# Kernel optimization log

Measured on AMD Instinct MI355X. Metric: run time of the kernel, lower is better.

## Reference

```python
import jax, jax.numpy as jnp
import numpy as np

B, H, D = 32, 64, 128          # batch (decode), indexer heads, head dim
PAGE, PAGES = 64, 128          # cache page size, pages per sequence
S = PAGE * PAGES               # max kv len = 8192
NUM_PAGES = B * PAGES          # 4096 pages total
TOPK = 2048
SCALE = float(D) ** -0.5
FILL = -1


def setup_inputs() -> dict:
    key = jax.random.key(0)
    ks = jax.random.split(key, 6)
    q = jax.random.normal(ks[0], (B, H, D), dtype=jnp.float32)
    k = jax.random.normal(ks[1], (B, D), dtype=jnp.float32)          # current-step key
    weights = jax.random.uniform(ks[2], (B, H), dtype=jnp.float32)   # per-head gates
    # fp8 cache emulated as quantized values (k_cache) x per-token scales (k_s_cache)
    k_cache = jax.random.normal(ks[3], (NUM_PAGES, PAGE, D), dtype=jnp.float32)
    k_s_cache = jax.random.uniform(ks[4], (NUM_PAGES, PAGE), minval=0.5, maxval=1.5, dtype=jnp.float32)
    kv_seqlens = jax.random.randint(ks[5], (B,), S // 2, S + 1, dtype=jnp.int32)
    block_offsets = jnp.arange(NUM_PAGES, dtype=jnp.int32).reshape(B, PAGES)
    return dict(q=q, k=k, weights=weights, k_cache=k_cache, k_s_cache=k_s_cache,
                kv_seqlens=kv_seqlens, block_offsets=block_offsets)


def reference(q, k, weights, k_cache, k_s_cache, kv_seqlens, block_offsets):
    # Gather paged cache per sequence and dequantize: [B, S, D]
    kv = k_cache[block_offsets].reshape(B, S, D) * k_s_cache[block_offsets].reshape(B, S, 1)
    pos = jnp.arange(S, dtype=jnp.int32)
    # Current step's key lives at position kv_len - 1
    cur = pos[None, :] == (kv_seqlens[:, None] - 1)
    kv = jnp.where(cur[..., None], k[:, None, :], kv)
    # Indexer score: sum_h w[b,h] * relu(q[b,h] . k[b,s]) * scale
    logits = jnp.einsum('bhd,bsd->bhs', q, kv) * SCALE
    scores = jnp.einsum('bh,bhs->bs', weights, jax.nn.relu(logits))  # [B, S]
    valid = pos[None, :] < kv_seqlens[:, None]
    scores = jnp.where(valid, scores, -jnp.inf)
    vals, idx = jax.lax.top_k(scores, TOPK)
    idx = jnp.where(jnp.isfinite(vals), idx, FILL).astype(jnp.int32)
    return idx, scores
```

## Files before the change

### kernel.cpp

```cpp
#include <hip/hip_runtime.h>
#include <hip/hip_bf16.h>
#include <math.h>

#define NB 32
#define NH 64
#define ND 128
#define PAGE_SZ 64
#define NPAGES 128
#define NS 8192
#define NTOPK 2048
#define QSCALE 0.08838834764831845f
#define NEG_SENTINEL -3.0e38f

typedef __attribute__((ext_vector_type(8))) short short8;
typedef __attribute__((ext_vector_type(4))) float f32x4;

static __device__ __forceinline__ unsigned pack2(float x, float y) {
    union { __hip_bfloat162 h; unsigned u; } c;
    c.h = __float22bfloat162_rn(make_float2(x, y));
    return c.u;
}

__global__ __launch_bounds__(256, 4) void score_kernel(
    const float* __restrict__ q,
    const float* __restrict__ kcur,
    const float* __restrict__ w,
    const float* __restrict__ kc,
    const float* __restrict__ ksc,
    const int*   __restrict__ kvlen,
    const int*   __restrict__ bo,
    float* __restrict__ scores_out)
{
    __shared__ __align__(16) unsigned short q_lds[64 * 128];
    __shared__ __align__(16) unsigned short kv_lds[2 * 64 * 128];
    __shared__ float w_lds[NH];

    const int b    = blockIdx.y;
    const int sb   = blockIdx.x;
    const int t    = threadIdx.x;
    const int wv   = t >> 6;
    const int lane = t & 63;
    const int len  = kvlen[b];
    const int cur  = len - 1;
    const int s_base = sb * 128;

    if (s_base >= len) {
        if (t < 128)
            scores_out[(size_t)b * NS + s_base + t] = NEG_SENTINEL;
        return;
    }

    const int l5 = lane & 31;

    float4 gA[8], gB[8];
#define LOADPG(P, G)                                                          \
    {                                                                         \
        int pg = bo[b * NPAGES + sb * 2 + (P)];                               \
        const float* kb = kc + (size_t)pg * (PAGE_SZ * ND);                   \
        _Pragma("unroll")                                                     \
        for (int i = 0; i < 8; ++i) {                                         \
            int tokL = wv * 16 + i * 2 + (lane >> 5);                         \
            bool iscur = (s_base + (P) * 64 + tokL) == cur;                   \
            const float* src = iscur                                          \
                ? (kcur + (size_t)b * ND + l5 * 4)                            \
                : (kb + wv * 2048 + i * 256 + lane * 4);                      \
            G[i] = *(const float4*)src;                                       \
        }                                                                     \
    }
    LOADPG(0, gA)
    LOADPG(1, gB)

    const int tokP = wv * 16 + (lane & 15);
    const int l4   = lane >> 4;
    float scP[2];
#pragma unroll
    for (int p = 0; p < 2; ++p) {
        int pg = bo[b * NPAGES + sb * 2 + p];
        bool iscur = (s_base + p * 64 + tokP) == cur;
        scP[p] = iscur ? 1.0f : ksc[pg * PAGE_SZ + tokP];
    }

    const float* qb = q + (size_t)b * NH * ND;
#pragma unroll
    for (int i = 0; i < 8; ++i) {
        int f = t + 256 * i;
        int row = f >> 5, d4 = f & 31;
        float4 v = *(const float4*)(qb + row * ND + d4 * 4);
        unsigned lo = pack2(v.x, v.y);
        unsigned hi = pack2(v.z, v.w);
        int ck = (d4 >> 1) ^ (row & 7);
        *(uint2*)(q_lds + row * 128 + (ck << 3) + (d4 & 1) * 4) = make_uint2(lo, hi);
    }
    if (t < NH) w_lds[t] = w[b * NH + t];

#define STAGE(G, P)                                                           \
    {                                                                         \
        _Pragma("unroll")                                                     \
        for (int i = 0; i < 8; ++i) {                                         \
            int tokL = wv * 16 + i * 2 + (lane >> 5);                         \
            unsigned lo = pack2(G[i].x, G[i].y);                              \
            unsigned hi = pack2(G[i].z, G[i].w);                              \
            int ch = (l5 >> 1) ^ (tokL & 7);                                  \
            *(uint2*)(kv_lds + (P) * 8192 + tokL * 128 + ch * 8 +             \
                      (lane & 1) * 4) = make_uint2(lo, hi);                   \
        }                                                                     \
    }
    STAGE(gA, 0)
    STAGE(gB, 1)
#undef LOADPG
#undef STAGE

    __syncthreads();

    float wgt[4][4];
#pragma unroll
    for (int hb = 0; hb < 4; ++hb)
#pragma unroll
        for (int r = 0; r < 4; ++r)
            wgt[hb][r] = w_lds[hb * 16 + l4 * 4 + r];

    const int arow = lane & 15;
    const int aswz = lane & 7;

#pragma unroll
    for (int p = 0; p < 2; ++p) {
        short8 bF[4];
#pragma unroll
        for (int ki = 0; ki < 4; ++ki) {
            int ch = (ki * 4 + l4) ^ (tokP & 7);
            bF[ki] = *(const short8*)(kv_lds + p * 8192 + tokP * 128 + ch * 8);
        }

        f32x4 acc[4];
#pragma unroll
        for (int hb = 0; hb < 4; ++hb) acc[hb] = (f32x4){0.f, 0.f, 0.f, 0.f};
#pragma unroll
        for (int ki = 0; ki < 4; ++ki) {
            const int ck = (ki * 4 + l4) ^ aswz;
#pragma unroll
            for (int hb = 0; hb < 4; ++hb) {
                short8 a = *(const short8*)(
                    q_lds + (hb * 16 + arow) * 128 + (ck << 3));
                acc[hb] = __builtin_amdgcn_mfma_f32_16x16x32_bf16(
                    a, bF[ki], acc[hb], 0, 0, 0);
            }
        }

        float part = 0.f;
#pragma unroll
        for (int hb = 0; hb < 4; ++hb)
#pragma unroll
            for (int r = 0; r < 4; ++r)
                part = fmaf(wgt[hb][r], fmaxf(acc[hb][r], 0.f), part);
        part += __shfl_xor(part, 16);
        part += __shfl_xor(part, 32);
        int sg = s_base + p * 64 + tokP;
        if (l4 == 0) {
            float val = part * (scP[p] * QSCALE);
            scores_out[(size_t)b * NS + sg] = (sg < len) ? val : NEG_SENTINEL;
        }
    }
}

static __device__ __forceinline__ void cex(unsigned &a, unsigned &b, bool desc) {
    unsigned lo = a < b ? a : b;
    unsigned hi = a < b ? b : a;
    a = desc ? hi : lo;
    b = desc ? lo : hi;
}

__global__ __launch_bounds__(256) void topk_sort(
    const float* __restrict__ scores,
    const int*   __restrict__ kvlen,
    unsigned* __restrict__ wsk)
{
    __shared__ unsigned keys[2048];
    const int b = blockIdx.y, c = blockIdx.x, t = threadIdx.x;
    unsigned* wrow = wsk + ((size_t)b * 4 + c) * 2048;

    if (c * 2048 >= kvlen[b]) {
#pragma unroll
        for (int r = 0; r < 8; ++r) wrow[t * 8 + r] = 0u;
        return;
    }

    const float* srow = scores + (size_t)b * NS + c * 2048;
    unsigned v[8];
    {
        float4 f0 = *(const float4*)(srow + t * 8);
        float4 f1 = *(const float4*)(srow + t * 8 + 4);
        float fv[8] = {f0.x, f0.y, f0.z, f0.w, f1.x, f1.y, f1.z, f1.w};
#pragma unroll
        for (int r = 0; r < 8; ++r) {
            int s = c * 2048 + t * 8 + r;
            float x = fv[r];
            v[r] = (x >= 0.f)
                 ? ((__float_as_uint(x) & 0xFFFFC000u) | (unsigned)(8192 - s))
                 : 0u;
        }
    }

    cex(v[0], v[1], true);  cex(v[2], v[3], false);
    cex(v[4], v[5], true);  cex(v[6], v[7], false);
    cex(v[0], v[2], true);  cex(v[1], v[3], true);
    cex(v[4], v[6], false); cex(v[5], v[7], false);
    cex(v[0], v[1], true);  cex(v[2], v[3], true);
    cex(v[4], v[5], false); cex(v[6], v[7], false);

    for (int k = 8; k <= 2048; k <<= 1) {
        const bool desc = (((unsigned)(t << 3)) & (unsigned)k) == 0u;
        for (int j = k >> 1; j >= 8; j >>= 1) {
            const int m = j >> 3;
            const bool keepHi = (((t & m) == 0) == desc);
            if (m < 64) {
#pragma unroll
                for (int r = 0; r < 8; ++r) {
                    unsigned o = __shfl_xor(v[r], m);
                    unsigned lo = v[r] < o ? v[r] : o;
                    unsigned hi = v[r] < o ? o : v[r];
                    v[r] = keepHi ? hi : lo;
                }
            } else {
                __syncthreads();
#pragma unroll
                for (int r = 0; r < 8; ++r) keys[t * 8 + r] = v[r];
                __syncthreads();
                const int pt = t ^ m;
#pragma unroll
                for (int r = 0; r < 8; ++r) {
                    unsigned o = keys[pt * 8 + r];
                    unsigned lo = v[r] < o ? v[r] : o;
                    unsigned hi = v[r] < o ? o : v[r];
                    v[r] = keepHi ? hi : lo;
                }
            }
        }
        cex(v[0], v[4], desc); cex(v[1], v[5], desc);
        cex(v[2], v[6], desc); cex(v[3], v[7], desc);
        cex(v[0], v[2], desc); cex(v[1], v[3], desc);
        cex(v[4], v[6], desc); cex(v[5], v[7], desc);
        cex(v[0], v[1], desc); cex(v[2], v[3], desc);
        cex(v[4], v[5], desc); cex(v[6], v[7], desc);
    }

#pragma unroll
    for (int r = 0; r < 8; ++r) wrow[t * 8 + r] = v[r];
}

__global__ __launch_bounds__(512) void topk_merge(
    const unsigned* __restrict__ wsk,
    int* __restrict__ idx_out)
{
    __shared__ unsigned keys[4096];
    const int b = blockIdx.x, t = threadIdx.x;
    const int g = t >> 8, tl = t & 255;
    const unsigned* base = wsk + (size_t)b * 4 * 2048;

    const unsigned* A = base + (2 * g) * 2048;
    const unsigned* B = base + (2 * g + 1) * 2048;
    unsigned v[8];
#pragma unroll
    for (int r = 0; r < 8; ++r) {
        int i = tl * 8 + r;
        unsigned a = A[i], bb = B[2047 - i];
        v[r] = a > bb ? a : bb;
    }
#pragma unroll
    for (int j = 1024; j >= 512; j >>= 1) {
        const int m = j >> 3;
        const bool keepHi = ((tl & m) == 0);
        __syncthreads();
#pragma unroll
        for (int r = 0; r < 8; ++r) keys[g * 2048 + tl * 8 + r] = v[r];
        __syncthreads();
        const int pt = tl ^ m;
#pragma unroll
        for (int r = 0; r < 8; ++r) {
            unsigned o = keys[g * 2048 + pt * 8 + r];
            unsigned lo = v[r] < o ? v[r] : o;
            unsigned hi = v[r] < o ? o : v[r];
            v[r] = keepHi ? hi : lo;
        }
    }
#pragma unroll
    for (int j = 256; j >= 8; j >>= 1) {
        const int m = j >> 3;
        const bool keepHi = ((tl & m) == 0);
#pragma unroll
        for (int r = 0; r < 8; ++r) {
            unsigned o = __shfl_xor(v[r], m);
            unsigned lo = v[r] < o ? v[r] : o;
            unsigned hi = v[r] < o ? o : v[r];
            v[r] = keepHi ? hi : lo;
        }
    }
    cex(v[0], v[4], true); cex(v[1], v[5], true);
    cex(v[2], v[6], true); cex(v[3], v[7], true);
    cex(v[0], v[2], true); cex(v[1], v[3], true);
    cex(v[4], v[6], true); cex(v[5], v[7], true);
    cex(v[0], v[1], true); cex(v[2], v[3], true);
    cex(v[4], v[5], true); cex(v[6], v[7], true);

    __syncthreads();
#pragma unroll
    for (int r = 0; r < 8; ++r) keys[g * 2048 + tl * 8 + r] = v[r];
    __syncthreads();

    unsigned u[4];
#pragma unroll
    for (int r = 0; r < 4; ++r) {
        int i = t * 4 + r;
        unsigned a = keys[i], bb = keys[2048 + 2047 - i];
        u[r] = a > bb ? a : bb;
    }
#pragma unroll
    for (int j = 1024; j >= 256; j >>= 1) {
        const int m = j >> 2;
        const bool keepHi = ((t & m) == 0);
        __syncthreads();
#pragma unroll
        for (int r = 0; r < 4; ++r) keys[t * 4 + r] = u[r];
        __syncthreads();
        const int pt = t ^ m;
#pragma unroll
        for (int r = 0; r < 4; ++r) {
            unsigned o = keys[pt * 4 + r];
            unsigned lo = u[r] < o ? u[r] : o;
            unsigned hi = u[r] < o ? o : u[r];
            u[r] = keepHi ? hi : lo;
        }
    }
#pragma unroll
    for (int j = 128; j >= 4; j >>= 1) {
        const int m = j >> 2;
        const bool keepHi = ((t & m) == 0);
#pragma unroll
        for (int r = 0; r < 4; ++r) {
            unsigned o = __shfl_xor(u[r], m);
            unsigned lo = u[r] < o ? u[r] : o;
            unsigned hi = u[r] < o ? o : u[r];
            u[r] = keepHi ? hi : lo;
        }
    }
    cex(u[0], u[2], true); cex(u[1], u[3], true);
    cex(u[0], u[1], true); cex(u[2], u[3], true);

#pragma unroll
    for (int r = 0; r < 4; ++r) {
        unsigned key = u[r];
        idx_out[b * NTOPK + t * 4 + r] =
            key ? (int)(8192u - (key & 0x3FFFu)) : -1;
    }
}

extern "C" void kernel_launch(void* const* d_in, const int* in_sizes, int n_in,
                              void* d_out, int out_size, void* d_ws, size_t ws_size,
                              hipStream_t stream)
{
    const float* q     = (const float*)d_in[0];
    const float* kcur  = (const float*)d_in[1];
    const float* w     = (const float*)d_in[2];
    const float* kc    = (const float*)d_in[3];
    const float* ksc   = (const float*)d_in[4];
    const int*   kvlen = (const int*)d_in[5];
    const int*   bo    = (const int*)d_in[6];

    int*      idx_out    = (int*)d_out;
    float*    scores_out = (float*)d_out + (size_t)NB * NTOPK;
    unsigned* wsk        = (unsigned*)d_ws;

    score_kernel<<<dim3(64, NB), 256, 0, stream>>>(q, kcur, w, kc, ksc, kvlen,
                                                   bo, scores_out);
    topk_sort<<<dim3(4, NB), 256, 0, stream>>>(scores_out, kvlen, wsk);
    topk_merge<<<NB, 512, 0, stream>>>(wsk, idx_out);
}
```

Measured before the change: 44.60 us.

## Single-buffer KV staging in score kernel, overlapping second page load with compute

Halves the KV shared-memory buffer and keeps one set of float4 registers instead of two. The second page's global load is issued before the first page's MFMA compute, then staged after an extra barrier. The goal is to cut LDS and register pressure so more blocks fit per CU, and to hide second-page load latency behind compute. It adds two more __syncthreads and reads the weights from LDS inside the compute loop instead of keeping them in registers.

```diff
diff --git a/kernel.cpp b/kernel.cpp
--- a/kernel.cpp
+++ b/kernel.cpp
@@ -32,7 +32,7 @@
     float* __restrict__ scores_out)
 {
     __shared__ __align__(16) unsigned short q_lds[64 * 128];
-    __shared__ __align__(16) unsigned short kv_lds[2 * 64 * 128];
+    __shared__ __align__(16) unsigned short kv_lds[64 * 128];
     __shared__ float w_lds[NH];
 
     const int b    = blockIdx.y;
@@ -50,35 +50,39 @@
         return;
     }
 
-    const int l5 = lane & 31;
-
-    float4 gA[8], gB[8];
-#define LOADPG(P, G)                                                          \
+    const int pg0 = bo[b * NPAGES + sb * 2];
+    const int pg1 = bo[b * NPAGES + sb * 2 + 1];
+
+    float4 G[8];
+#define LOADPG(PG, P)                                                         \
     {                                                                         \
-        int pg = bo[b * NPAGES + sb * 2 + (P)];                               \
-        const float* kb = kc + (size_t)pg * (PAGE_SZ * ND);                   \
+        const float* kb = kc + (size_t)(PG) * (PAGE_SZ * ND);                 \
         _Pragma("unroll")                                                     \
         for (int i = 0; i < 8; ++i) {                                         \
-            int tokL = wv * 16 + i * 2 + (lane >> 5);                         \
+            int f = t + 256 * i;                                              \
+            int tokL = f >> 5;                                                \
             bool iscur = (s_base + (P) * 64 + tokL) == cur;                   \
             const float* src = iscur                                          \
-                ? (kcur + (size_t)b * ND + l5 * 4)                            \
-                : (kb + wv * 2048 + i * 256 + lane * 4);                      \
+                ? (kcur + (size_t)b * ND + (f & 31) * 4)                      \
+                : (kb + (size_t)f * 4);                                       \
             G[i] = *(const float4*)src;                                       \
         }                                                                     \
     }
-    LOADPG(0, gA)
-    LOADPG(1, gB)
-
-    const int tokP = wv * 16 + (lane & 15);
-    const int l4   = lane >> 4;
-    float scP[2];
-#pragma unroll
-    for (int p = 0; p < 2; ++p) {
-        int pg = bo[b * NPAGES + sb * 2 + p];
-        bool iscur = (s_base + p * 64 + tokP) == cur;
-        scP[p] = iscur ? 1.0f : ksc[pg * PAGE_SZ + tokP];
-    }
+#define STAGE_KV()                                                            \
+    {                                                                         \
+        _Pragma("unroll")                                                     \
+        for (int i = 0; i < 8; ++i) {                                         \
+            int f = t + 256 * i;                                              \
+            int tokL = f >> 5, d4 = f & 31;                                   \
+            unsigned lo = pack2(G[i].x, G[i].y);                              \
+            unsigned hi = pack2(G[i].z, G[i].w);                              \
+            int ck = (d4 >> 1) ^ (tokL & 7);                                  \
+            *(uint2*)(kv_lds + tokL * 128 + (ck << 3) + (d4 & 1) * 4) =       \
+                make_uint2(lo, hi);                                           \
+        }                                                                     \
+    }
+
+    LOADPG(pg0, 0)
 
     const float* qb = q + (size_t)b * NH * ND;
 #pragma unroll
@@ -93,73 +97,73 @@
     }
     if (t < NH) w_lds[t] = w[b * NH + t];
 
-#define STAGE(G, P)                                                           \
-    {                                                                         \
-        _Pragma("unroll")                                                     \
-        for (int i = 0; i < 8; ++i) {                                         \
-            int tokL = wv * 16 + i * 2 + (lane >> 5);                         \
-            unsigned lo = pack2(G[i].x, G[i].y);                              \
-            unsigned hi = pack2(G[i].z, G[i].w);                              \
-            int ch = (l5 >> 1) ^ (tokL & 7);                                  \
-            *(uint2*)(kv_lds + (P) * 8192 + tokL * 128 + ch * 8 +             \
-                      (lane & 1) * 4) = make_uint2(lo, hi);                   \
-        }                                                                     \
-    }
-    STAGE(gA, 0)
-    STAGE(gB, 1)
-#undef LOADPG
-#undef STAGE
-
-    __syncthreads();
-
-    float wgt[4][4];
-#pragma unroll
-    for (int hb = 0; hb < 4; ++hb)
-#pragma unroll
-        for (int r = 0; r < 4; ++r)
-            wgt[hb][r] = w_lds[hb * 16 + l4 * 4 + r];
+    const int tokP = wv * 16 + (lane & 15);
+    const int l4   = lane >> 4;
+    const float scP0 = ((s_base + tokP) == cur) ? 1.0f
+                       : ksc[pg0 * PAGE_SZ + tokP];
+    const float scP1 = ((s_base + 64 + tokP) == cur) ? 1.0f
+                       : ksc[pg1 * PAGE_SZ + tokP];
+
+    STAGE_KV()
+    LOADPG(pg1, 1)
+
+    __syncthreads();
 
     const int arow = lane & 15;
     const int aswz = lane & 7;
 
-#pragma unroll
-    for (int p = 0; p < 2; ++p) {
-        short8 bF[4];
-#pragma unroll
-        for (int ki = 0; ki < 4; ++ki) {
-            int ch = (ki * 4 + l4) ^ (tokP & 7);
-            bF[ki] = *(const short8*)(kv_lds + p * 8192 + tokP * 128 + ch * 8);
-        }
-
-        f32x4 acc[4];
-#pragma unroll
-        for (int hb = 0; hb < 4; ++hb) acc[hb] = (f32x4){0.f, 0.f, 0.f, 0.f};
-#pragma unroll
-        for (int ki = 0; ki < 4; ++ki) {
-            const int ck = (ki * 4 + l4) ^ aswz;
-#pragma unroll
-            for (int hb = 0; hb < 4; ++hb) {
-                short8 a = *(const short8*)(
-                    q_lds + (hb * 16 + arow) * 128 + (ck << 3));
-                acc[hb] = __builtin_amdgcn_mfma_f32_16x16x32_bf16(
-                    a, bF[ki], acc[hb], 0, 0, 0);
-            }
-        }
-
-        float part = 0.f;
-#pragma unroll
-        for (int hb = 0; hb < 4; ++hb)
-#pragma unroll
-            for (int r = 0; r < 4; ++r)
-                part = fmaf(wgt[hb][r], fmaxf(acc[hb][r], 0.f), part);
-        part += __shfl_xor(part, 16);
-        part += __shfl_xor(part, 32);
-        int sg = s_base + p * 64 + tokP;
-        if (l4 == 0) {
-            float val = part * (scP[p] * QSCALE);
-            scores_out[(size_t)b * NS + sg] = (sg < len) ? val : NEG_SENTINEL;
-        }
-    }
+#define COMPUTE_PAGE(SCP, SOFF)                                               \
+    {                                                                         \
+        short8 bF[4];                                                         \
+        _Pragma("unroll")                                                     \
+        for (int ki = 0; ki < 4; ++ki) {                                      \
+            int ch = (ki * 4 + l4) ^ (tokP & 7);                              \
+            bF[ki] = *(const short8*)(kv_lds + tokP * 128 + (ch << 3));       \
+        }                                                                     \
+        f32x4 acc[4];                                                         \
+        _Pragma("unroll")                                                     \
+        for (int hb = 0; hb < 4; ++hb) acc[hb] = (f32x4){0.f, 0.f, 0.f, 0.f};\
+        _Pragma("unroll")                                                     \
+        for (int ki = 0; ki < 4; ++ki) {                                      \
+            const int ck = (ki * 4 + l4) ^ aswz;                              \
+            _Pragma("unroll")                                                 \
+            for (int hb = 0; hb < 4; ++hb) {                                  \
+                short8 a = *(const short8*)(                                  \
+                    q_lds + (hb * 16 + arow) * 128 + (ck << 3));              \
+                acc[hb] = __builtin_amdgcn_mfma_f32_16x16x32_bf16(            \
+                    a, bF[ki], acc[hb], 0, 0, 0);                             \
+            }                                                                 \
+        }                                                                     \
+        float part = 0.f;                                                     \
+        _Pragma("unroll")                                                     \
+        for (int hb = 0; hb < 4; ++hb)                                        \
+            _Pragma("unroll")                                                 \
+            for (int r = 0; r < 4; ++r)                                       \
+                part = fmaf(w_lds[hb * 16 + l4 * 4 + r],                      \
+                            fmaxf(acc[hb][r], 0.f), part);                    \
+        part += __shfl_xor(part, 16);                                         \
+        part += __shfl_xor(part, 32);                                         \
+        int sg = s_base + (SOFF) + tokP;                                      \
+        if (l4 == 0) {                                                        \
+            float val = part * ((SCP) * QSCALE);                              \
+            scores_out[(size_t)b * NS + sg] =                                 \
+                (sg < len) ? val : NEG_SENTINEL;                              \
+        }                                                                     \
+    }
+
+    COMPUTE_PAGE(scP0, 0)
+
+    __syncthreads();
+
+    STAGE_KV()
+
+    __syncthreads();
+
+    COMPUTE_PAGE(scP1, 64)
+
+#undef LOADPG
+#undef STAGE_KV
+#undef COMPUTE_PAGE
 }
 
 static __device__ __forceinline__ void cex(unsigned &a, unsigned &b, bool desc) {
```

After: 41.39 us. -7.2%, faster.
